# Optimization experiments

Measured on AMD Instinct MI355X. Metric: run time of the kernel, lower is better.

The kernel has to match this reference:

```python
import jax, jax.numpy as jnp
import numpy as np

DIM = 1024
H = 16
DH = DIM // H  # 64
B = 2
T = 2048
LEFT, RIGHT = 128, 128  # attention_window
CAUSAL = True
SCALE = 1.0 / float(np.sqrt(DH))


def rotate_half(x):
    x1, x2 = jnp.split(x, 2, axis=-1)
    return jnp.concatenate((-x2, x1), axis=-1)


def apply_rotary_pos_emb(pos, t):
    # pos: [b, t, dh] -> [b, 1, t, dh]; t: [b, h, t, dh]
    pos = pos[:, None]
    return t * jnp.cos(pos) + rotate_half(t) * jnp.sin(pos)


def setup_inputs() -> dict:
    key = jax.random.key(0)
    ks = jax.random.split(key, 6)
    s = 1.0 / np.sqrt(DIM)
    x = jax.random.normal(ks[0], (B, T, DIM), dtype=jnp.float32)
    attention_mask = jnp.ones((T, T), dtype=bool)
    rotary_emb = jax.random.normal(ks[1], (B, T, DH), dtype=jnp.float32)
    Wq = jax.random.normal(ks[2], (DIM, DIM), dtype=jnp.float32) * s
    Wk = jax.random.normal(ks[3], (DIM, DIM), dtype=jnp.float32) * s
    Wv = jax.random.normal(ks[4], (DIM, DIM), dtype=jnp.float32) * s
    Wo = jax.random.normal(ks[5], (DIM, DIM), dtype=jnp.float32) * s
    return {"x": x, "attention_mask": attention_mask, "rotary_emb": rotary_emb,
            "Wq": Wq, "Wk": Wk, "Wv": Wv, "Wo": Wo}


def _build_mask(attention_mask):
    # i = key/column index, j = query/row index (matches torch code)
    i = jnp.arange(T)[None, :]
    j = jnp.arange(T)[:, None]
    mask = (i >= j - LEFT) & (i <= j + RIGHT)  # sliding window
    if CAUSAL:
        mask = mask & (i <= j)  # tril
    return attention_mask & mask  # [T, T]


def reference(x, attention_mask, rotary_emb, Wq, Wk, Wv, Wo):
    b, t, d = x.shape
    # QKV projections (nn.Linear: x @ W.T), split heads: b t (h dh) -> b h t dh
    def proj(W):
        return (x @ W.T).reshape(b, t, H, DH).transpose(0, 2, 1, 3)
    q, k, v = proj(Wq), proj(Wk), proj(Wv)
    q = apply_rotary_pos_emb(rotary_emb, q)
    k = apply_rotary_pos_emb(rotary_emb, k)
    mask = _build_mask(attention_mask)  # [T, T]
    scores = jnp.einsum('bhqd,bhkd->bhqk', q, k) * SCALE
    neg = jnp.asarray(-1e9, scores.dtype)
    scores = jnp.where(mask, scores, neg)
    attn = jax.nn.softmax(scores, axis=-1)
    out = jnp.einsum('bhqk,bhkd->bhqd', attn, v)
    out = out.transpose(0, 2, 1, 3).reshape(b, t, d)  # b h t dh -> b t (h dh)
    return out @ Wo.T
```

## Files before the change

### kernel.cpp

```cpp
#include <hip/hip_runtime.h>
#include <hip/hip_bf16.h>
#include <cstdint>

#define DIMD 1024
#define NH 16
#define DHD 64
#define BB 2
#define TT 2048
#define MROWS (BB * TT)

typedef unsigned short u16;
typedef unsigned int u32;
typedef __attribute__((ext_vector_type(8))) __bf16 bf16x8;
typedef __attribute__((ext_vector_type(4))) float f32x4;

__device__ __forceinline__ u16 f2bf(float f) {
    union { float f; unsigned int i; } v; v.f = f;
    unsigned int u = v.i;
    unsigned int r = (u + 0x7fffu + ((u >> 16) & 1u)) >> 16;
    return (u16)r;
}
__device__ __forceinline__ int4 pack8(const float4& a, const float4& b) {
    union { int4 v; u16 u[8]; } t;
    t.u[0] = f2bf(a.x); t.u[1] = f2bf(a.y); t.u[2] = f2bf(a.z); t.u[3] = f2bf(a.w);
    t.u[4] = f2bf(b.x); t.u[5] = f2bf(b.y); t.u[6] = f2bf(b.z); t.u[7] = f2bf(b.w);
    return t.v;
}
__device__ __forceinline__ void gl_lds16(const u16* g, u16* l) {
    __builtin_amdgcn_global_load_lds(
        (const __attribute__((address_space(1))) u32*)g,
        (__attribute__((address_space(3))) u32*)l, 16, 0, 0);
}

__global__ __launch_bounds__(256) void convert_all(const float* __restrict__ x,
                                                   const float* __restrict__ Wq,
                                                   const float* __restrict__ Wk,
                                                   const float* __restrict__ Wv,
                                                   const float* __restrict__ Wo,
                                                   u16* __restrict__ xb,
                                                   u16* __restrict__ wqkv,
                                                   u16* __restrict__ wob) {
    int t = blockIdx.x * 256 + threadIdx.x;
    const float* src; u16* dst; int rel;
    if (t < 524288)      { src = x;  dst = xb;             rel = t; }
    else if (t < 655360) { src = Wq; dst = wqkv;           rel = t - 524288; }
    else if (t < 786432) { src = Wk; dst = wqkv + 1048576; rel = t - 655360; }
    else if (t < 917504) { src = Wv; dst = wqkv + 2097152; rel = t - 786432; }
    else                 { src = Wo; dst = wob;            rel = t - 917504; }
    size_t e = (size_t)rel * 8;
    float4 a = *(const float4*)(src + e);
    float4 b = *(const float4*)(src + e + 4);
    *(int4*)(dst + e) = pack8(a, b);
}

__global__ __launch_bounds__(256) void gemm_qkv(const u16* __restrict__ xb,
                                                const u16* __restrict__ wqkv,
                                                u16* __restrict__ qb,
                                                u16* __restrict__ kb,
                                                u16* __restrict__ vbT,
                                                const float* __restrict__ rot) {
    constexpr int Kd = 1024;
    __shared__ u16 As[2][128 * 32];
    __shared__ u16 Bs[2][128 * 32];

    const int tid  = threadIdx.x;
    const int lane = tid & 63;
    const int w    = tid >> 6;
    const int m0   = blockIdx.y * 128;
    const int n0   = blockIdx.x * 128;

    const u16* Ag = xb   + (size_t)(m0 + 32 * w + (lane >> 2)) * Kd + (lane & 3) * 8;
    const u16* Bg = wqkv + (size_t)(n0 + 32 * w + (lane >> 2)) * Kd + (lane & 3) * 8;
    const int loff0 = (32 * w) * 32;
    const int loff1 = (32 * w + 16) * 32;

    const int r16  = lane & 15;
    const int quad = lane >> 4;
    const int q8   = quad * 8;
    const int wm   = (w >> 1) * 64;
    const int wn   = (w & 1) * 64;

    f32x4 acc[4][4];
#pragma unroll
    for (int i = 0; i < 4; i++)
#pragma unroll
        for (int j = 0; j < 4; j++) acc[i][j] = f32x4{0.f, 0.f, 0.f, 0.f};

#pragma unroll 1
    for (int k0 = 0; k0 < Kd; k0 += 64) {
        __syncthreads();
        gl_lds16(Ag + k0, &As[0][loff0]);
        gl_lds16(Ag + 16 * Kd + k0, &As[0][loff1]);
        gl_lds16(Bg + k0, &Bs[0][loff0]);
        gl_lds16(Bg + 16 * Kd + k0, &Bs[0][loff1]);
        gl_lds16(Ag + k0 + 32, &As[1][loff0]);
        gl_lds16(Ag + 16 * Kd + k0 + 32, &As[1][loff1]);
        gl_lds16(Bg + k0 + 32, &Bs[1][loff0]);
        gl_lds16(Bg + 16 * Kd + k0 + 32, &Bs[1][loff1]);
        __syncthreads();

#pragma unroll
        for (int p = 0; p < 2; p++) {
            bf16x8 af[4], bfr[4];
#pragma unroll
            for (int i = 0; i < 4; i++)
                af[i] = *(const bf16x8*)&As[p][(wm + i * 16 + r16) * 32 + q8];
#pragma unroll
            for (int j = 0; j < 4; j++)
                bfr[j] = *(const bf16x8*)&Bs[p][(wn + j * 16 + r16) * 32 + q8];
#pragma unroll
            for (int mi = 0; mi < 4; mi++)
#pragma unroll
                for (int ni = 0; ni < 4; ni++)
                    acc[mi][ni] = __builtin_amdgcn_mfma_f32_16x16x32_bf16(
                        af[mi], bfr[ni], acc[mi][ni], 0, 0, 0);
        }
    }

    const int wsel = n0 >> 10;
    const int nloc = (n0 & 1023) + wn;

    if (wsel < 2) {
        u16* C = (wsel == 0) ? qb : kb;
#pragma unroll
        for (int mi = 0; mi < 4; mi++)
#pragma unroll
            for (int r = 0; r < 4; r++) {
                int row = m0 + wm + mi * 16 + quad * 4 + r;
#pragma unroll
                for (int ni = 0; ni < 2; ni++) {
                    int d = ni * 16 + r16;
                    float s0, c0, s1, c1;
                    __sincosf(rot[row * DHD + d], &s0, &c0);
                    __sincosf(rot[row * DHD + d + 32], &s1, &c1);
                    float x0 = acc[mi][ni][r], x1 = acc[mi][ni + 2][r];
                    C[(size_t)row * DIMD + nloc + d]      = f2bf(x0 * c0 - x1 * s0);
                    C[(size_t)row * DIMD + nloc + d + 32] = f2bf(x1 * c1 + x0 * s1);
                }
            }
    } else {
#pragma unroll
        for (int mi = 0; mi < 4; mi++)
#pragma unroll
            for (int ni = 0; ni < 4; ni++)
#pragma unroll
                for (int r = 0; r < 4; r++) {
                    int row = m0 + wm + mi * 16 + quad * 4 + r;
                    int b   = row >> 11;
                    int t   = row & (TT - 1);
                    int col = nloc + ni * 16 + r16;
                    int h   = col >> 6;
                    int d   = col & 63;
                    vbT[((size_t)(b * NH + h) * DHD + d) * TT + t] =
                        f2bf(acc[mi][ni][r]);
                }
    }
}

__global__ __launch_bounds__(256) void attn_kernel(const u16* __restrict__ Q,
                                                   const u16* __restrict__ K,
                                                   const u16* __restrict__ vbT,
                                                   u16* __restrict__ O) {
    constexpr int LDK = 72;
    constexpr int LDV = 200;
    __shared__ u16 Ks[192 * LDK];
    __shared__ u16 Qs[64 * LDK];
    __shared__ u16 VTs[64 * LDV];

    const int tid = threadIdx.x;
    const int L   = tid & 63;
    const int w   = tid >> 6;
    const int b   = blockIdx.z;
    const int h   = blockIdx.y;
    const int q0  = blockIdx.x * 64;
    const int kstart = q0 - 128;

    for (int i = tid; i < 512; i += 256) {
        int qr = i >> 3, c = (i & 7) * 8;
        *(int4*)&Qs[qr * LDK + c] =
            *(const int4*)&Q[(size_t)(b * TT + q0 + qr) * DIMD + h * DHD + c];
    }
    for (int i = tid; i < 1536; i += 256) {
        int kr = i >> 3, c = (i & 7) * 8;
        int kk = kstart + kr;
        int4 val = make_int4(0, 0, 0, 0);
        if (kk >= 0)
            val = *(const int4*)&K[(size_t)(b * TT + kk) * DIMD + h * DHD + c];
        *(int4*)&Ks[kr * LDK + c] = val;
    }
    for (int i = tid; i < 1536; i += 256) {
        int d = i / 24;
        int c = (i % 24) * 8;
        int kk = kstart + c;
        int4 val = make_int4(0, 0, 0, 0);
        if (kk >= 0)
            val = *(const int4*)&vbT[((size_t)(b * NH + h) * DHD + d) * TT + kk];
        *(int4*)&VTs[d * LDV + c] = val;
    }
    __syncthreads();

    const int r16  = L & 15;
    const int quad = L >> 4;
    const int q8   = quad * 8;

    bf16x8 aq0 = *(const bf16x8*)&Qs[(w * 16 + r16) * LDK + q8];
    bf16x8 aq1 = *(const bf16x8*)&Qs[(w * 16 + r16) * LDK + 32 + q8];

    float st[12][4];
    float rmax[4] = {-1e30f, -1e30f, -1e30f, -1e30f};
    const float SC = 0.125f;

#pragma unroll
    for (int kt = 0; kt < 12; kt++) {
        bf16x8 bk0 = *(const bf16x8*)&Ks[(kt * 16 + r16) * LDK + q8];
        bf16x8 bk1 = *(const bf16x8*)&Ks[(kt * 16 + r16) * LDK + 32 + q8];
        f32x4 s = f32x4{0.f, 0.f, 0.f, 0.f};
        s = __builtin_amdgcn_mfma_f32_16x16x32_bf16(aq0, bk0, s, 0, 0, 0);
        s = __builtin_amdgcn_mfma_f32_16x16x32_bf16(aq1, bk1, s, 0, 0, 0);
        int ka = kstart + kt * 16 + r16;
#pragma unroll
        for (int r = 0; r < 4; r++) {
            int qa = q0 + w * 16 + quad * 4 + r;
            float sv = s[r] * SC;
            bool ok = (ka >= 0) && (ka <= qa) && (ka >= qa - 128);
            sv = ok ? sv : -1e30f;
            st[kt][r] = sv;
            rmax[r] = fmaxf(rmax[r], sv);
        }
    }
#pragma unroll
    for (int off = 8; off >= 1; off >>= 1)
#pragma unroll
        for (int r = 0; r < 4; r++)
            rmax[r] = fmaxf(rmax[r], __shfl_xor(rmax[r], off, 64));

    __syncthreads();

    u16* Ps = &Ks[w * 16 * LDV];
    float rsum[4] = {0.f, 0.f, 0.f, 0.f};
#pragma unroll
    for (int kt = 0; kt < 12; kt++)
#pragma unroll
        for (int r = 0; r < 4; r++) {
            float p = __expf(st[kt][r] - rmax[r]);
            rsum[r] += p;
            Ps[(quad * 4 + r) * LDV + kt * 16 + r16] = f2bf(p);
        }
#pragma unroll
    for (int off = 8; off >= 1; off >>= 1)
#pragma unroll
        for (int r = 0; r < 4; r++)
            rsum[r] += __shfl_xor(rsum[r], off, 64);
    float rinv[4];
#pragma unroll
    for (int r = 0; r < 4; r++) rinv[r] = 1.0f / rsum[r];

    __syncthreads();

    bf16x8 pa[6];
#pragma unroll
    for (int kc = 0; kc < 6; kc++)
        pa[kc] = *(const bf16x8*)&Ps[r16 * LDV + kc * 32 + q8];

#pragma unroll
    for (int nt = 0; nt < 4; nt++) {
        f32x4 acc = f32x4{0.f, 0.f, 0.f, 0.f};
#pragma unroll
        for (int kc = 0; kc < 6; kc++) {
            bf16x8 bv = *(const bf16x8*)&VTs[(nt * 16 + r16) * LDV + kc * 32 + q8];
            acc = __builtin_amdgcn_mfma_f32_16x16x32_bf16(pa[kc], bv, acc, 0, 0, 0);
        }
#pragma unroll
        for (int r = 0; r < 4; r++) {
            int qa = q0 + w * 16 + quad * 4 + r;
            O[(size_t)(b * TT + qa) * DIMD + h * DHD + nt * 16 + r16] =
                f2bf(acc[r] * rinv[r]);
        }
    }
}

__global__ __launch_bounds__(256) void gemm_out(const u16* __restrict__ A,
                                                const u16* __restrict__ Wb,
                                                float* __restrict__ C) {
    constexpr int Kd = 1024, Nd = 1024;
    __shared__ u16 As[64 * 32];
    __shared__ u16 Bs[128 * 32];

    const int tid  = threadIdx.x;
    const int lane = tid & 63;
    const int w    = tid >> 6;
    const int m0   = blockIdx.y * 64;
    const int n0   = blockIdx.x * 128;

    const u16* Ag = A  + (size_t)(m0 + 16 * w + (lane >> 2)) * Kd + (lane & 3) * 8;
    const u16* Bg = Wb + (size_t)(n0 + 32 * w + (lane >> 2)) * Kd + (lane & 3) * 8;
    u16* Al  = &As[(16 * w) * 32];
    u16* Bl0 = &Bs[(32 * w) * 32];
    u16* Bl1 = &Bs[(32 * w + 16) * 32];

    const int r16  = lane & 15;
    const int quad = lane >> 4;
    const int q8   = quad * 8;
    const int cb   = (w >> 1) * 64 + (w & 1) * 16;

    f32x4 acc[4][2];
#pragma unroll
    for (int i = 0; i < 4; i++)
#pragma unroll
        for (int j = 0; j < 2; j++) acc[i][j] = f32x4{0.f, 0.f, 0.f, 0.f};

#pragma unroll 1
    for (int k0 = 0; k0 < Kd; k0 += 32) {
        __syncthreads();
        gl_lds16(Ag + k0, Al);
        gl_lds16(Bg + k0, Bl0);
        gl_lds16(Bg + 16 * Kd + k0, Bl1);
        __syncthreads();

        bf16x8 af[4], bfr[2];
#pragma unroll
        for (int i = 0; i < 4; i++)
            af[i] = *(const bf16x8*)&As[(i * 16 + r16) * 32 + q8];
#pragma unroll
        for (int j = 0; j < 2; j++)
            bfr[j] = *(const bf16x8*)&Bs[(cb + j * 32 + r16) * 32 + q8];
#pragma unroll
        for (int mi = 0; mi < 4; mi++)
#pragma unroll
            for (int ni = 0; ni < 2; ni++)
                acc[mi][ni] = __builtin_amdgcn_mfma_f32_16x16x32_bf16(
                    af[mi], bfr[ni], acc[mi][ni], 0, 0, 0);
    }

#pragma unroll
    for (int mi = 0; mi < 4; mi++)
#pragma unroll
        for (int j = 0; j < 2; j++)
#pragma unroll
            for (int r = 0; r < 4; r++) {
                int row = m0 + mi * 16 + quad * 4 + r;
                C[(size_t)row * Nd + n0 + cb + j * 32 + r16] = acc[mi][j][r];
            }
}

extern "C" void kernel_launch(void* const* d_in, const int* in_sizes, int n_in,
                              void* d_out, int out_size, void* d_ws, size_t ws_size,
                              hipStream_t stream) {
    const float* x   = (const float*)d_in[0];
    const float* rot = (const float*)d_in[2];
    const float* Wq  = (const float*)d_in[3];
    const float* Wk  = (const float*)d_in[4];
    const float* Wv  = (const float*)d_in[5];
    const float* Wo  = (const float*)d_in[6];
    float* out = (float*)d_out;

    u16* xb   = (u16*)d_ws;
    u16* wqkv = xb + 4194304;
    u16* wob  = wqkv + 3145728;
    u16* qb   = wob + 1048576;
    u16* kb   = qb + 4194304;
    u16* vbT  = kb + 4194304;
    u16* ab   = vbT + 4194304;

    convert_all<<<4096, 256, 0, stream>>>(x, Wq, Wk, Wv, Wo, xb, wqkv, wob);
    gemm_qkv<<<dim3(3 * DIMD / 128, MROWS / 128), 256, 0, stream>>>(
        xb, wqkv, qb, kb, vbT, rot);
    attn_kernel<<<dim3(TT / 64, NH, BB), 256, 0, stream>>>(qb, kb, vbT, ab);
    gemm_out<<<dim3(DIMD / 128, MROWS / 64), 256, 0, stream>>>(ab, wob, out);
}
```

Measured before the change: 189.4 us.

## Remap GEMM blocks for XCD locality, halve QKV K-step, trim attention syncs

Both GEMMs now use a 1D grid. Block indices are remapped so that blocks landing on the same XCD (bid&7) share weight columns, which is meant to improve L2 reuse. The QKV GEMM drops its 64-wide K step with two LDS buffers in favour of a single 32-wide tile per iteration. That halves LDS use but doubles the number of barrier pairs. In attention, Q fragments are loaded straight from global memory into registers and P gets a dedicated LDS buffer, which removes one __syncthreads but adds LDS footprint.

```diff
diff --git a/kernel.cpp b/kernel.cpp
--- a/kernel.cpp
+++ b/kernel.cpp
@@ -60,19 +60,25 @@
                                                 u16* __restrict__ vbT,
                                                 const float* __restrict__ rot) {
     constexpr int Kd = 1024;
-    __shared__ u16 As[2][128 * 32];
-    __shared__ u16 Bs[2][128 * 32];
+    __shared__ u16 As[128 * 32];
+    __shared__ u16 Bs[128 * 32];
+
+    const int bid = blockIdx.x;
+    const int xcd = bid & 7;
+    const int kk  = bid >> 3;
+    const int m0  = (kk / 3) * 128;
+    const int n0  = ((kk % 3) * 8 + xcd) * 128;
 
     const int tid  = threadIdx.x;
     const int lane = tid & 63;
     const int w    = tid >> 6;
-    const int m0   = blockIdx.y * 128;
-    const int n0   = blockIdx.x * 128;
 
     const u16* Ag = xb   + (size_t)(m0 + 32 * w + (lane >> 2)) * Kd + (lane & 3) * 8;
     const u16* Bg = wqkv + (size_t)(n0 + 32 * w + (lane >> 2)) * Kd + (lane & 3) * 8;
-    const int loff0 = (32 * w) * 32;
-    const int loff1 = (32 * w + 16) * 32;
+    u16* Al0 = &As[(32 * w) * 32];
+    u16* Al1 = &As[(32 * w + 16) * 32];
+    u16* Bl0 = &Bs[(32 * w) * 32];
+    u16* Bl1 = &Bs[(32 * w + 16) * 32];
 
     const int r16  = lane & 15;
     const int quad = lane >> 4;
@@ -87,34 +93,27 @@
         for (int j = 0; j < 4; j++) acc[i][j] = f32x4{0.f, 0.f, 0.f, 0.f};
 
 #pragma unroll 1
-    for (int k0 = 0; k0 < Kd; k0 += 64) {
+    for (int k0 = 0; k0 < Kd; k0 += 32) {
         __syncthreads();
-        gl_lds16(Ag + k0, &As[0][loff0]);
-        gl_lds16(Ag + 16 * Kd + k0, &As[0][loff1]);
-        gl_lds16(Bg + k0, &Bs[0][loff0]);
-        gl_lds16(Bg + 16 * Kd + k0, &Bs[0][loff1]);
-        gl_lds16(Ag + k0 + 32, &As[1][loff0]);
-        gl_lds16(Ag + 16 * Kd + k0 + 32, &As[1][loff1]);
-        gl_lds16(Bg + k0 + 32, &Bs[1][loff0]);
-        gl_lds16(Bg + 16 * Kd + k0 + 32, &Bs[1][loff1]);
+        gl_lds16(Ag + k0, Al0);
+        gl_lds16(Ag + 16 * Kd + k0, Al1);
+        gl_lds16(Bg + k0, Bl0);
+        gl_lds16(Bg + 16 * Kd + k0, Bl1);
         __syncthreads();
 
-#pragma unroll
-        for (int p = 0; p < 2; p++) {
-            bf16x8 af[4], bfr[4];
-#pragma unroll
-            for (int i = 0; i < 4; i++)
-                af[i] = *(const bf16x8*)&As[p][(wm + i * 16 + r16) * 32 + q8];
-#pragma unroll
-            for (int j = 0; j < 4; j++)
-                bfr[j] = *(const bf16x8*)&Bs[p][(wn + j * 16 + r16) * 32 + q8];
-#pragma unroll
-            for (int mi = 0; mi < 4; mi++)
-#pragma unroll
-                for (int ni = 0; ni < 4; ni++)
-                    acc[mi][ni] = __builtin_amdgcn_mfma_f32_16x16x32_bf16(
-                        af[mi], bfr[ni], acc[mi][ni], 0, 0, 0);
-        }
+        bf16x8 af[4], bfr[4];
+#pragma unroll
+        for (int i = 0; i < 4; i++)
+            af[i] = *(const bf16x8*)&As[(wm + i * 16 + r16) * 32 + q8];
+#pragma unroll
+        for (int j = 0; j < 4; j++)
+            bfr[j] = *(const bf16x8*)&Bs[(wn + j * 16 + r16) * 32 + q8];
+#pragma unroll
+        for (int mi = 0; mi < 4; mi++)
+#pragma unroll
+            for (int ni = 0; ni < 4; ni++)
+                acc[mi][ni] = __builtin_amdgcn_mfma_f32_16x16x32_bf16(
+                    af[mi], bfr[ni], acc[mi][ni], 0, 0, 0);
     }
 
     const int wsel = n0 >> 10;
@@ -164,8 +163,8 @@
     constexpr int LDK = 72;
     constexpr int LDV = 200;
     __shared__ u16 Ks[192 * LDK];
-    __shared__ u16 Qs[64 * LDK];
     __shared__ u16 VTs[64 * LDV];
+    __shared__ u16 Ps[4 * 16 * LDV];
 
     const int tid = threadIdx.x;
     const int L   = tid & 63;
@@ -175,11 +174,6 @@
     const int q0  = blockIdx.x * 64;
     const int kstart = q0 - 128;
 
-    for (int i = tid; i < 512; i += 256) {
-        int qr = i >> 3, c = (i & 7) * 8;
-        *(int4*)&Qs[qr * LDK + c] =
-            *(const int4*)&Q[(size_t)(b * TT + q0 + qr) * DIMD + h * DHD + c];
-    }
     for (int i = tid; i < 1536; i += 256) {
         int kr = i >> 3, c = (i & 7) * 8;
         int kk = kstart + kr;
@@ -197,14 +191,16 @@
             val = *(const int4*)&vbT[((size_t)(b * NH + h) * DHD + d) * TT + kk];
         *(int4*)&VTs[d * LDV + c] = val;
     }
-    __syncthreads();
 
     const int r16  = L & 15;
     const int quad = L >> 4;
     const int q8   = quad * 8;
 
-    bf16x8 aq0 = *(const bf16x8*)&Qs[(w * 16 + r16) * LDK + q8];
-    bf16x8 aq1 = *(const bf16x8*)&Qs[(w * 16 + r16) * LDK + 32 + q8];
+    const size_t qrow = (size_t)(b * TT + q0 + w * 16 + r16) * DIMD + h * DHD;
+    bf16x8 aq0 = *(const bf16x8*)&Q[qrow + q8];
+    bf16x8 aq1 = *(const bf16x8*)&Q[qrow + 32 + q8];
+
+    __syncthreads();
 
     float st[12][4];
     float rmax[4] = {-1e30f, -1e30f, -1e30f, -1e30f};
@@ -234,9 +230,7 @@
         for (int r = 0; r < 4; r++)
             rmax[r] = fmaxf(rmax[r], __shfl_xor(rmax[r], off, 64));
 
-    __syncthreads();
-
-    u16* Ps = &Ks[w * 16 * LDV];
+    u16* Pw = &Ps[w * 16 * LDV];
     float rsum[4] = {0.f, 0.f, 0.f, 0.f};
 #pragma unroll
     for (int kt = 0; kt < 12; kt++)
@@ -244,7 +238,7 @@
         for (int r = 0; r < 4; r++) {
             float p = __expf(st[kt][r] - rmax[r]);
             rsum[r] += p;
-            Ps[(quad * 4 + r) * LDV + kt * 16 + r16] = f2bf(p);
+            Pw[(quad * 4 + r) * LDV + kt * 16 + r16] = f2bf(p);
         }
 #pragma unroll
     for (int off = 8; off >= 1; off >>= 1)
@@ -260,7 +254,7 @@
     bf16x8 pa[6];
 #pragma unroll
     for (int kc = 0; kc < 6; kc++)
-        pa[kc] = *(const bf16x8*)&Ps[r16 * LDV + kc * 32 + q8];
+        pa[kc] = *(const bf16x8*)&Pw[r16 * LDV + kc * 32 + q8];
 
 #pragma unroll
     for (int nt = 0; nt < 4; nt++) {
@@ -286,11 +280,13 @@
     __shared__ u16 As[64 * 32];
     __shared__ u16 Bs[128 * 32];
 
+    const int bid = blockIdx.x;
+    const int n0  = (bid & 7) * 128;
+    const int m0  = (bid >> 3) * 64;
+
     const int tid  = threadIdx.x;
     const int lane = tid & 63;
     const int w    = tid >> 6;
-    const int m0   = blockIdx.y * 64;
-    const int n0   = blockIdx.x * 128;
 
     const u16* Ag = A  + (size_t)(m0 + 16 * w + (lane >> 2)) * Kd + (lane & 3) * 8;
     const u16* Bg = Wb + (size_t)(n0 + 32 * w + (lane >> 2)) * Kd + (lane & 3) * 8;
@@ -363,8 +359,7 @@
     u16* ab   = vbT + 4194304;
 
     convert_all<<<4096, 256, 0, stream>>>(x, Wq, Wk, Wv, Wo, xb, wqkv, wob);
-    gemm_qkv<<<dim3(3 * DIMD / 128, MROWS / 128), 256, 0, stream>>>(
-        xb, wqkv, qb, kb, vbT, rot);
+    gemm_qkv<<<768, 256, 0, stream>>>(xb, wqkv, qb, kb, vbT, rot);
     attn_kernel<<<dim3(TT / 64, NH, BB), 256, 0, stream>>>(qb, kb, vbT, ab);
-    gemm_out<<<dim3(DIMD / 128, MROWS / 64), 256, 0, stream>>>(ab, wob, out);
-}
+    gemm_out<<<512, 256, 0, stream>>>(ab, wob, out);
+}
```

Result: slower. 193.3 us (+2.0%).

## Software-pipeline GEMM tiles through registers with LDS double buffering; trim attention syncs

Applied to the files above, without the earlier changes.

Both GEMMs drop direct global-to-LDS loads and instead load the next K-slice into registers while MFMAs run on the current LDS buffer, then write it to the other buffer. This gives one barrier per half-step instead of two syncs around a blocking load. The attention kernel loads Q fragments straight from global memory into registers and gives P its own LDS buffer, which removes a barrier. The cost is more VGPRs and LDS use, which may lower occupancy.

```diff
diff --git a/kernel.cpp b/kernel.cpp
--- a/kernel.cpp
+++ b/kernel.cpp
@@ -25,11 +25,6 @@
     t.u[0] = f2bf(a.x); t.u[1] = f2bf(a.y); t.u[2] = f2bf(a.z); t.u[3] = f2bf(a.w);
     t.u[4] = f2bf(b.x); t.u[5] = f2bf(b.y); t.u[6] = f2bf(b.z); t.u[7] = f2bf(b.w);
     return t.v;
-}
-__device__ __forceinline__ void gl_lds16(const u16* g, u16* l) {
-    __builtin_amdgcn_global_load_lds(
-        (const __attribute__((address_space(1))) u32*)g,
-        (__attribute__((address_space(3))) u32*)l, 16, 0, 0);
 }
 
 __global__ __launch_bounds__(256) void convert_all(const float* __restrict__ x,
@@ -71,8 +66,8 @@
 
     const u16* Ag = xb   + (size_t)(m0 + 32 * w + (lane >> 2)) * Kd + (lane & 3) * 8;
     const u16* Bg = wqkv + (size_t)(n0 + 32 * w + (lane >> 2)) * Kd + (lane & 3) * 8;
-    const int loff0 = (32 * w) * 32;
-    const int loff1 = (32 * w + 16) * 32;
+    const int soff0 = (32 * w + (lane >> 2)) * 32 + (lane & 3) * 8;
+    const int soff1 = soff0 + 16 * 32;
 
     const int r16  = lane & 15;
     const int quad = lane >> 4;
@@ -86,34 +81,50 @@
 #pragma unroll
         for (int j = 0; j < 4; j++) acc[i][j] = f32x4{0.f, 0.f, 0.f, 0.f};
 
+    int4 a0, a1, b0, b1;
+    auto loadregs = [&](int k) {
+        a0 = *(const int4*)(Ag + k);
+        a1 = *(const int4*)(Ag + 16 * Kd + k);
+        b0 = *(const int4*)(Bg + k);
+        b1 = *(const int4*)(Bg + 16 * Kd + k);
+    };
+    auto writebuf = [&](int buf) {
+        *(int4*)&As[buf][soff0] = a0;
+        *(int4*)&As[buf][soff1] = a1;
+        *(int4*)&Bs[buf][soff0] = b0;
+        *(int4*)&Bs[buf][soff1] = b1;
+    };
+    auto compute = [&](int buf) {
+        bf16x8 af[4], bfr[4];
+#pragma unroll
+        for (int i = 0; i < 4; i++)
+            af[i] = *(const bf16x8*)&As[buf][(wm + i * 16 + r16) * 32 + q8];
+#pragma unroll
+        for (int j = 0; j < 4; j++)
+            bfr[j] = *(const bf16x8*)&Bs[buf][(wn + j * 16 + r16) * 32 + q8];
+#pragma unroll
+        for (int mi = 0; mi < 4; mi++)
+#pragma unroll
+            for (int ni = 0; ni < 4; ni++)
+                acc[mi][ni] = __builtin_amdgcn_mfma_f32_16x16x32_bf16(
+                    af[mi], bfr[ni], acc[mi][ni], 0, 0, 0);
+    };
+
+    loadregs(0);
+    writebuf(0);
+    __syncthreads();
+
 #pragma unroll 1
     for (int k0 = 0; k0 < Kd; k0 += 64) {
+        loadregs(k0 + 32);
+        compute(0);
+        writebuf(1);
         __syncthreads();
-        gl_lds16(Ag + k0, &As[0][loff0]);
-        gl_lds16(Ag + 16 * Kd + k0, &As[0][loff1]);
-        gl_lds16(Bg + k0, &Bs[0][loff0]);
-        gl_lds16(Bg + 16 * Kd + k0, &Bs[0][loff1]);
-        gl_lds16(Ag + k0 + 32, &As[1][loff0]);
-        gl_lds16(Ag + 16 * Kd + k0 + 32, &As[1][loff1]);
-        gl_lds16(Bg + k0 + 32, &Bs[1][loff0]);
-        gl_lds16(Bg + 16 * Kd + k0 + 32, &Bs[1][loff1]);
-        __syncthreads();
-
-#pragma unroll
-        for (int p = 0; p < 2; p++) {
-            bf16x8 af[4], bfr[4];
-#pragma unroll
-            for (int i = 0; i < 4; i++)
-                af[i] = *(const bf16x8*)&As[p][(wm + i * 16 + r16) * 32 + q8];
-#pragma unroll
-            for (int j = 0; j < 4; j++)
-                bfr[j] = *(const bf16x8*)&Bs[p][(wn + j * 16 + r16) * 32 + q8];
-#pragma unroll
-            for (int mi = 0; mi < 4; mi++)
-#pragma unroll
-                for (int ni = 0; ni < 4; ni++)
-                    acc[mi][ni] = __builtin_amdgcn_mfma_f32_16x16x32_bf16(
-                        af[mi], bfr[ni], acc[mi][ni], 0, 0, 0);
+        if (k0 + 64 < Kd) loadregs(k0 + 64);
+        compute(1);
+        if (k0 + 64 < Kd) {
+            writebuf(0);
+            __syncthreads();
         }
     }
 
@@ -164,8 +175,8 @@
     constexpr int LDK = 72;
     constexpr int LDV = 200;
     __shared__ u16 Ks[192 * LDK];
-    __shared__ u16 Qs[64 * LDK];
     __shared__ u16 VTs[64 * LDV];
+    __shared__ u16 Ps[4 * 16 * LDV];
 
     const int tid = threadIdx.x;
     const int L   = tid & 63;
@@ -175,11 +186,6 @@
     const int q0  = blockIdx.x * 64;
     const int kstart = q0 - 128;
 
-    for (int i = tid; i < 512; i += 256) {
-        int qr = i >> 3, c = (i & 7) * 8;
-        *(int4*)&Qs[qr * LDK + c] =
-            *(const int4*)&Q[(size_t)(b * TT + q0 + qr) * DIMD + h * DHD + c];
-    }
     for (int i = tid; i < 1536; i += 256) {
         int kr = i >> 3, c = (i & 7) * 8;
         int kk = kstart + kr;
@@ -197,14 +203,16 @@
             val = *(const int4*)&vbT[((size_t)(b * NH + h) * DHD + d) * TT + kk];
         *(int4*)&VTs[d * LDV + c] = val;
     }
-    __syncthreads();
 
     const int r16  = L & 15;
     const int quad = L >> 4;
     const int q8   = quad * 8;
 
-    bf16x8 aq0 = *(const bf16x8*)&Qs[(w * 16 + r16) * LDK + q8];
-    bf16x8 aq1 = *(const bf16x8*)&Qs[(w * 16 + r16) * LDK + 32 + q8];
+    const size_t qrow = (size_t)(b * TT + q0 + w * 16 + r16) * DIMD + h * DHD;
+    bf16x8 aq0 = *(const bf16x8*)&Q[qrow + q8];
+    bf16x8 aq1 = *(const bf16x8*)&Q[qrow + 32 + q8];
+
+    __syncthreads();
 
     float st[12][4];
     float rmax[4] = {-1e30f, -1e30f, -1e30f, -1e30f};
@@ -234,9 +242,7 @@
         for (int r = 0; r < 4; r++)
             rmax[r] = fmaxf(rmax[r], __shfl_xor(rmax[r], off, 64));
 
-    __syncthreads();
-
-    u16* Ps = &Ks[w * 16 * LDV];
+    u16* Pw = &Ps[w * 16 * LDV];
     float rsum[4] = {0.f, 0.f, 0.f, 0.f};
 #pragma unroll
     for (int kt = 0; kt < 12; kt++)
@@ -244,7 +250,7 @@
         for (int r = 0; r < 4; r++) {
             float p = __expf(st[kt][r] - rmax[r]);
             rsum[r] += p;
-            Ps[(quad * 4 + r) * LDV + kt * 16 + r16] = f2bf(p);
+            Pw[(quad * 4 + r) * LDV + kt * 16 + r16] = f2bf(p);
         }
 #pragma unroll
     for (int off = 8; off >= 1; off >>= 1)
@@ -260,7 +266,7 @@
     bf16x8 pa[6];
 #pragma unroll
     for (int kc = 0; kc < 6; kc++)
-        pa[kc] = *(const bf16x8*)&Ps[r16 * LDV + kc * 32 + q8];
+        pa[kc] = *(const bf16x8*)&Pw[r16 * LDV + kc * 32 + q8];
 
 #pragma unroll
     for (int nt = 0; nt < 4; nt++) {
@@ -283,8 +289,8 @@
                                                 const u16* __restrict__ Wb,
                                                 float* __restrict__ C) {
     constexpr int Kd = 1024, Nd = 1024;
-    __shared__ u16 As[64 * 32];
-    __shared__ u16 Bs[128 * 32];
+    __shared__ u16 As[2][64 * 32];
+    __shared__ u16 Bs[2][128 * 32];
 
     const int tid  = threadIdx.x;
     const int lane = tid & 63;
@@ -294,9 +300,9 @@
 
     const u16* Ag = A  + (size_t)(m0 + 16 * w + (lane >> 2)) * Kd + (lane & 3) * 8;
     const u16* Bg = Wb + (size_t)(n0 + 32 * w + (lane >> 2)) * Kd + (lane & 3) * 8;
-    u16* Al  = &As[(16 * w) * 32];
-    u16* Bl0 = &Bs[(32 * w) * 32];
-    u16* Bl1 = &Bs[(32 * w + 16) * 32];
+    const int aoff  = (16 * w + (lane >> 2)) * 32 + (lane & 3) * 8;
+    const int boff0 = (32 * w + (lane >> 2)) * 32 + (lane & 3) * 8;
+    const int boff1 = boff0 + 16 * 32;
 
     const int r16  = lane & 15;
     const int quad = lane >> 4;
@@ -309,27 +315,49 @@
 #pragma unroll
         for (int j = 0; j < 2; j++) acc[i][j] = f32x4{0.f, 0.f, 0.f, 0.f};
 
-#pragma unroll 1
-    for (int k0 = 0; k0 < Kd; k0 += 32) {
-        __syncthreads();
-        gl_lds16(Ag + k0, Al);
-        gl_lds16(Bg + k0, Bl0);
-        gl_lds16(Bg + 16 * Kd + k0, Bl1);
-        __syncthreads();
-
+    int4 a0, b0, b1;
+    auto loadregs = [&](int k) {
+        a0 = *(const int4*)(Ag + k);
+        b0 = *(const int4*)(Bg + k);
+        b1 = *(const int4*)(Bg + 16 * Kd + k);
+    };
+    auto writebuf = [&](int buf) {
+        *(int4*)&As[buf][aoff]  = a0;
+        *(int4*)&Bs[buf][boff0] = b0;
+        *(int4*)&Bs[buf][boff1] = b1;
+    };
+    auto compute = [&](int buf) {
         bf16x8 af[4], bfr[2];
 #pragma unroll
         for (int i = 0; i < 4; i++)
-            af[i] = *(const bf16x8*)&As[(i * 16 + r16) * 32 + q8];
+            af[i] = *(const bf16x8*)&As[buf][(i * 16 + r16) * 32 + q8];
 #pragma unroll
         for (int j = 0; j < 2; j++)
-            bfr[j] = *(const bf16x8*)&Bs[(cb + j * 32 + r16) * 32 + q8];
+            bfr[j] = *(const bf16x8*)&Bs[buf][(cb + j * 32 + r16) * 32 + q8];
 #pragma unroll
         for (int mi = 0; mi < 4; mi++)
 #pragma unroll
             for (int ni = 0; ni < 2; ni++)
                 acc[mi][ni] = __builtin_amdgcn_mfma_f32_16x16x32_bf16(
                     af[mi], bfr[ni], acc[mi][ni], 0, 0, 0);
+    };
+
+    loadregs(0);
+    writebuf(0);
+    __syncthreads();
+
+#pragma unroll 1
+    for (int k0 = 0; k0 < Kd; k0 += 64) {
+        loadregs(k0 + 32);
+        compute(0);
+        writebuf(1);
+        __syncthreads();
+        if (k0 + 64 < Kd) loadregs(k0 + 64);
+        compute(1);
+        if (k0 + 64 < Kd) {
+            writebuf(0);
+            __syncthreads();
+        }
     }
 
 #pragma unroll
```

Result: faster. 170.0 us (-10.3%).
